# Kernel optimization log

Hardware: AMD Instinct MI355X
Metric: run time of the kernel (lower is better)

The kernel has to match this reference:

```python
import jax, jax.numpy as jnp
import numpy as np

EMBED_DIM = 1024
NUM_HEADS = 16
HEAD_DIM = EMBED_DIM // NUM_HEADS
LN_EPS = 1e-5


def setup_inputs() -> dict:
    key = jax.random.key(0)
    ks = jax.random.split(key, 12)
    B, SQ, SKV, E = 2, 1024, 4096, EMBED_DIM
    s = 1.0 / np.sqrt(E)
    return {
        "query": jax.random.normal(ks[0], (B, SQ, E), jnp.float32),
        "key_value": jax.random.normal(ks[1], (B, SKV, E), jnp.float32),
        "key_value_mask": jax.random.randint(ks[2], (B, SKV), 0, 2, jnp.int32),
        "Wq": jax.random.normal(ks[3], (E, E), jnp.float32) * s,
        "bq": jnp.zeros((E,), jnp.float32),
        "Wk": jax.random.normal(ks[4], (E, E), jnp.float32) * s,
        "bk": jnp.zeros((E,), jnp.float32),
        "Wv": jax.random.normal(ks[5], (E, E), jnp.float32) * s,
        "bv": jnp.zeros((E,), jnp.float32),
        "Wo": jax.random.normal(ks[6], (E, E), jnp.float32) * s,
        "bo": jnp.zeros((E,), jnp.float32),
        "ln_gamma": jnp.ones((E,), jnp.float32),
        "ln_beta": jnp.zeros((E,), jnp.float32),
    }


def reference(query, key_value, key_value_mask, Wq, bq, Wk, bk, Wv, bv, Wo, bo, ln_gamma, ln_beta):
    B, SQ, E = query.shape
    SKV = key_value.shape[1]
    H, D = NUM_HEADS, HEAD_DIM
    # projections (dropout is eval-mode identity)
    q = (query @ Wq.T + bq).reshape(B, SQ, H, D).transpose(0, 2, 1, 3)      # b h sq d
    k = (key_value @ Wk.T + bk).reshape(B, SKV, H, D).transpose(0, 2, 1, 3)  # b h skv d
    v = (key_value @ Wv.T + bv).reshape(B, SKV, H, D).transpose(0, 2, 1, 3)
    scale = jnp.sqrt(jnp.asarray(D, q.dtype))
    scores = jnp.einsum('bhqd,bhkd->bhqk', q, k) / scale                     # b h sq skv
    mask = (key_value_mask != 0)[:, None, None, :]                           # b 1 1 skv
    scores = jnp.where(mask, scores, jnp.asarray(-jnp.inf, scores.dtype))
    attn = jax.nn.softmax(scores, axis=-1)
    out = jnp.einsum('bhqk,bhkd->bhqd', attn, v)
    out = out.transpose(0, 2, 1, 3).reshape(B, SQ, E)
    out = out @ Wo.T + bo
    # post-LN residual
    x = query + out
    mu = jnp.mean(x, axis=-1, keepdims=True)
    var = jnp.mean(jnp.square(x - mu), axis=-1, keepdims=True)
    return (x - mu) * jax.lax.rsqrt(var + LN_EPS) * ln_gamma + ln_beta
```

## Files before the change

kernel.cpp:

```cpp
#include <hip/hip_runtime.h>
#include <cstdint>


typedef __bf16 bf16x8_t  __attribute__((ext_vector_type(8)));
typedef float  f32x4_t   __attribute__((ext_vector_type(4)));
typedef float  f32x16_t  __attribute__((ext_vector_type(16)));

#define E_DIM 1024
#define NH    16
#define HD    64
#define SCALE_L2E 0.1803368804f

__device__ __forceinline__ unsigned short f32_bf16(float f) {
    union { float f; unsigned int u; } v; v.f = f;
    unsigned int u = v.u;
    unsigned int r = (u + 0x7fffu + ((u >> 16) & 1u)) >> 16;
    return (unsigned short)r;
}

__device__ __forceinline__ unsigned pack_bf16(float a, float b) {
    __bf16 x = (__bf16)a, y = (__bf16)b;
    unsigned short ux = __builtin_bit_cast(unsigned short, x);
    unsigned short uy = __builtin_bit_cast(unsigned short, y);
    return (unsigned)ux | ((unsigned)uy << 16);
}

__device__ __forceinline__ void gld16(const unsigned short* g, unsigned short* l) {
    __builtin_amdgcn_global_load_lds(
        (const __attribute__((address_space(1))) unsigned int*)g,
        (__attribute__((address_space(3))) unsigned int*)l, 16, 0, 0);
}

__device__ __forceinline__ bf16x8_t ld16g(const unsigned short* p) {
    union { uint4 u; bf16x8_t f; } v;
    v.u = *reinterpret_cast<const uint4*>(p);
    return v.f;
}

__global__ void cast_all(const float* __restrict__ q, const float* __restrict__ kv,
                         const float* __restrict__ wq, const float* __restrict__ wk,
                         const float* __restrict__ wv, const float* __restrict__ wo,
                         unsigned short* __restrict__ Xq, unsigned short* __restrict__ Xkv,
                         unsigned short* __restrict__ Wqb, unsigned short* __restrict__ Wkb,
                         unsigned short* __restrict__ Wvb, unsigned short* __restrict__ Wob,
                         const int* __restrict__ msk, float* __restrict__ Sub) {
    __shared__ int red[4];
    if (blockIdx.x >= 14336) {
        int b = blockIdx.x - 14336, t = threadIdx.x;
        int s = 0;
#pragma unroll
        for (int k = 0; k < 16; k++) s += (msk[b * 4096 + k * 256 + t] != 0);
#pragma unroll
        for (int off = 32; off >= 1; off >>= 1) s += __shfl_xor(s, off, 64);
        if ((t & 63) == 0) red[t >> 6] = s;
        __syncthreads();
        if (t == 0)
            Sub[b] = (float)(4096 - (red[0] + red[1] + red[2] + red[3]));
        return;
    }
    long i = (long)blockIdx.x * 256 + threadIdx.x;
    const float* src; unsigned short* dst; long off;
    if (i < 2621440) {
        if (i < 524288) { src = q;  dst = Xq;  off = i; }
        else            { src = kv; dst = Xkv; off = i - 524288; }
    } else {
        long j = i - 2621440;
        int w = (int)(j >> 18); off = j & 262143;
        src = (w == 0) ? wq : (w == 1) ? wk : (w == 2) ? wv : wo;
        dst = (w == 0) ? Wqb : (w == 1) ? Wkb : (w == 2) ? Wvb : Wob;
    }
    float4 v = reinterpret_cast<const float4*>(src)[off];
    ushort4 o;
    o.x = f32_bf16(v.x); o.y = f32_bf16(v.y);
    o.z = f32_bf16(v.z); o.w = f32_bf16(v.w);
    reinterpret_cast<ushort4*>(dst)[off] = o;
}

#define BK 64

__global__ __launch_bounds__(256) void gemm_q(
    const unsigned short* __restrict__ A,
    const unsigned short* __restrict__ W,
    const float* __restrict__ bias,
    unsigned short* __restrict__ out)
{
    __shared__ __align__(16) unsigned short As[64 * BK];
    __shared__ __align__(16) unsigned short Bs[128 * BK];
    int tid  = threadIdx.x;
    int m0   = blockIdx.y * 64;
    int n0   = blockIdx.x * 128;
    int lane = tid & 63;
    int wvu  = __builtin_amdgcn_readfirstlane(tid >> 6);
    int l15  = lane & 15, quad = lane >> 4, x7 = l15 & 7;
    int wm   = ((tid >> 6) >> 1) * 32, wn = ((tid >> 6) & 1) * 64;

    f32x4_t acc[2][4];
#pragma unroll
    for (int i = 0; i < 2; i++)
#pragma unroll
        for (int j = 0; j < 4; j++) acc[i][j] = (f32x4_t)(0.f);

    for (int k0 = 0; k0 < 1024; k0 += BK) {
        __syncthreads();
#pragma unroll
        for (int i = 0; i < 2; i++) {
            int s = (i * 4 + wvu) * 64 + lane;
            int row = s >> 3, pcol = ((s & 7) ^ (row & 7)) << 3;
            gld16(&A[(long)(m0 + row) * 1024 + k0 + pcol], &As[(i * 4 + wvu) * 512]);
        }
#pragma unroll
        for (int i = 0; i < 4; i++) {
            int s = (i * 4 + wvu) * 64 + lane;
            int row = s >> 3, pcol = ((s & 7) ^ (row & 7)) << 3;
            gld16(&W[(long)(n0 + row) * 1024 + k0 + pcol], &Bs[(i * 4 + wvu) * 512]);
        }
        __syncthreads();
        const char* Ab = (const char*)As;
        const char* Bb = (const char*)Bs;
#pragma unroll
        for (int ks = 0; ks < 2; ks++) {
            int pos = (((ks << 2) + quad) ^ x7) << 4;
            bf16x8_t af[2], bf[4];
#pragma unroll
            for (int mi = 0; mi < 2; mi++)
                af[mi] = *reinterpret_cast<const bf16x8_t*>(
                    Ab + (wm + mi * 16 + l15) * 128 + pos);
#pragma unroll
            for (int ni = 0; ni < 4; ni++)
                bf[ni] = *reinterpret_cast<const bf16x8_t*>(
                    Bb + (wn + ni * 16 + l15) * 128 + pos);
#pragma unroll
            for (int mi = 0; mi < 2; mi++)
#pragma unroll
                for (int ni = 0; ni < 4; ni++)
                    acc[mi][ni] = __builtin_amdgcn_mfma_f32_16x16x32_bf16(
                        af[mi], bf[ni], acc[mi][ni], 0, 0, 0);
        }
    }
#pragma unroll
    for (int mi = 0; mi < 2; mi++)
#pragma unroll
        for (int ni = 0; ni < 4; ni++) {
            int n = n0 + wn + ni * 16 + l15;
            float bv = bias[n];
            int h = n >> 6, d = n & 63;
#pragma unroll
            for (int r = 0; r < 4; r++) {
                int mg = m0 + wm + mi * 16 + quad * 4 + r;
                int b = mg >> 10, s = mg & 1023;
                out[(((b * NH + h) << 10) + s) * HD + d] =
                    f32_bf16((acc[mi][ni][r] + bv) * SCALE_L2E);
            }
        }
}

__global__ __launch_bounds__(256) void gemm_kv(
    const unsigned short* __restrict__ A,
    const unsigned short* __restrict__ Wk,
    const unsigned short* __restrict__ Wv,
    const float* __restrict__ bk,
    const float* __restrict__ bv,
    unsigned short* __restrict__ Kout,
    unsigned short* __restrict__ Vout,
    const int* __restrict__ kvm)
{
    __shared__ __align__(16) unsigned short As[128 * BK];
    __shared__ __align__(16) unsigned short Bs[128 * BK];
    int tid  = threadIdx.x;
    int bx   = blockIdx.x;
    int isV  = bx >= 8;
    int m0   = blockIdx.y * 128;
    int n0   = (bx & 7) * 128;
    const unsigned short* W = isV ? Wv : Wk;
    const float* bias = isV ? bv : bk;
    int lane = tid & 63;
    int wvu  = __builtin_amdgcn_readfirstlane(tid >> 6);
    int l15  = lane & 15, quad = lane >> 4, x7 = l15 & 7;
    int wm   = ((tid >> 6) >> 1) * 64, wn = ((tid >> 6) & 1) * 64;

    f32x4_t acc[4][4];
#pragma unroll
    for (int i = 0; i < 4; i++)
#pragma unroll
        for (int j = 0; j < 4; j++) acc[i][j] = (f32x4_t)(0.f);

    for (int k0 = 0; k0 < 1024; k0 += BK) {
        __syncthreads();
#pragma unroll
        for (int i = 0; i < 4; i++) {
            int s = (i * 4 + wvu) * 64 + lane;
            int row = s >> 3, pcol = ((s & 7) ^ (row & 7)) << 3;
            gld16(&A[(long)(m0 + row) * 1024 + k0 + pcol], &As[(i * 4 + wvu) * 512]);
            gld16(&W[(long)(n0 + row) * 1024 + k0 + pcol], &Bs[(i * 4 + wvu) * 512]);
        }
        __syncthreads();
        const char* Ab = (const char*)As;
        const char* Bb = (const char*)Bs;
#pragma unroll
        for (int ks = 0; ks < 2; ks++) {
            int pos = (((ks << 2) + quad) ^ x7) << 4;
            bf16x8_t af[4], bf[4];
#pragma unroll
            for (int mi = 0; mi < 4; mi++)
                af[mi] = *reinterpret_cast<const bf16x8_t*>(
                    Ab + (wm + mi * 16 + l15) * 128 + pos);
#pragma unroll
            for (int ni = 0; ni < 4; ni++)
                bf[ni] = *reinterpret_cast<const bf16x8_t*>(
                    Bb + (wn + ni * 16 + l15) * 128 + pos);
#pragma unroll
            for (int mi = 0; mi < 4; mi++)
#pragma unroll
                for (int ni = 0; ni < 4; ni++)
                    acc[mi][ni] = __builtin_amdgcn_mfma_f32_16x16x32_bf16(
                        af[mi], bf[ni], acc[mi][ni], 0, 0, 0);
        }
    }
    int4 mk[4];
#pragma unroll
    for (int mi = 0; mi < 4; mi++) {
        int mg0 = m0 + wm + mi * 16 + quad * 4;
        mk[mi] = *reinterpret_cast<const int4*>(&kvm[mg0]);
    }
    if (!isV) {
#pragma unroll
        for (int mi = 0; mi < 4; mi++)
#pragma unroll
            for (int ni = 0; ni < 4; ni++) {
                int n = n0 + wn + ni * 16 + l15;
                float bvv = bias[n];
                int h = n >> 6, d = n & 63;
#pragma unroll
                for (int r = 0; r < 4; r++) {
                    int mg = m0 + wm + mi * 16 + quad * 4 + r;
                    int b = mg >> 12, s = mg & 4095;
                    unsigned short val = (&mk[mi].x)[r]
                        ? f32_bf16(acc[mi][ni][r] + bvv) : (unsigned short)0;
                    Kout[(((b * NH + h) << 12) + s) * HD + d] = val;
                }
            }
    } else {
#pragma unroll
        for (int mi = 0; mi < 4; mi++)
#pragma unroll
            for (int ni = 0; ni < 4; ni++) {
                int n = n0 + wn + ni * 16 + l15;
                float bvv = bias[n];
                int h = n >> 6, d = n & 63;
                int mg0 = m0 + wm + mi * 16 + quad * 4;
                int b = mg0 >> 12, s = mg0 & 4095;
                ushort4 w;
                w.x = mk[mi].x ? f32_bf16(acc[mi][ni][0] + bvv) : (unsigned short)0;
                w.y = mk[mi].y ? f32_bf16(acc[mi][ni][1] + bvv) : (unsigned short)0;
                w.z = mk[mi].z ? f32_bf16(acc[mi][ni][2] + bvv) : (unsigned short)0;
                w.w = mk[mi].w ? f32_bf16(acc[mi][ni][3] + bvv) : (unsigned short)0;
                *reinterpret_cast<ushort4*>(
                    &Vout[(((b * NH + h) * HD + d) << 12) + s]) = w;
            }
    }
}

__global__ __launch_bounds__(256) void gemm_oproj(
    const unsigned short* __restrict__ A,
    const unsigned short* __restrict__ W,
    const float* __restrict__ bias,
    const float* __restrict__ resid,
    float* __restrict__ xout)
{
    __shared__ __align__(16) unsigned short As[64 * BK];
    __shared__ __align__(16) unsigned short Bs[128 * BK];
    int tid  = threadIdx.x;
    int m0   = blockIdx.y * 64;
    int n0   = blockIdx.x * 128;
    int lane = tid & 63;
    int wvu  = __builtin_amdgcn_readfirstlane(tid >> 6);
    int l15  = lane & 15, quad = lane >> 4, x7 = l15 & 7;
    int wm   = ((tid >> 6) >> 1) * 32, wn = ((tid >> 6) & 1) * 64;

    f32x4_t acc[2][4];
#pragma unroll
    for (int i = 0; i < 2; i++)
#pragma unroll
        for (int j = 0; j < 4; j++) acc[i][j] = (f32x4_t)(0.f);

    for (int k0 = 0; k0 < 1024; k0 += BK) {
        __syncthreads();
#pragma unroll
        for (int i = 0; i < 2; i++) {
            int s = (i * 4 + wvu) * 64 + lane;
            int row = s >> 3, pcol = ((s & 7) ^ (row & 7)) << 3;
            gld16(&A[(long)(m0 + row) * 1024 + k0 + pcol], &As[(i * 4 + wvu) * 512]);
        }
#pragma unroll
        for (int i = 0; i < 4; i++) {
            int s = (i * 4 + wvu) * 64 + lane;
            int row = s >> 3, pcol = ((s & 7) ^ (row & 7)) << 3;
            gld16(&W[(long)(n0 + row) * 1024 + k0 + pcol], &Bs[(i * 4 + wvu) * 512]);
        }
        __syncthreads();
        const char* Ab = (const char*)As;
        const char* Bb = (const char*)Bs;
#pragma unroll
        for (int ks = 0; ks < 2; ks++) {
            int pos = (((ks << 2) + quad) ^ x7) << 4;
            bf16x8_t af[2], bf[4];
#pragma unroll
            for (int mi = 0; mi < 2; mi++)
                af[mi] = *reinterpret_cast<const bf16x8_t*>(
                    Ab + (wm + mi * 16 + l15) * 128 + pos);
#pragma unroll
            for (int ni = 0; ni < 4; ni++)
                bf[ni] = *reinterpret_cast<const bf16x8_t*>(
                    Bb + (wn + ni * 16 + l15) * 128 + pos);
#pragma unroll
            for (int mi = 0; mi < 2; mi++)
#pragma unroll
                for (int ni = 0; ni < 4; ni++)
                    acc[mi][ni] = __builtin_amdgcn_mfma_f32_16x16x32_bf16(
                        af[mi], bf[ni], acc[mi][ni], 0, 0, 0);
        }
    }
#pragma unroll
    for (int mi = 0; mi < 2; mi++)
#pragma unroll
        for (int ni = 0; ni < 4; ni++) {
            int n = n0 + wn + ni * 16 + l15;
            float bv = bias[n];
#pragma unroll
            for (int r = 0; r < 4; r++) {
                int mg = m0 + wm + mi * 16 + quad * 4 + r;
                xout[mg * 1024 + n] = acc[mi][ni][r] + bv + resid[mg * 1024 + n];
            }
        }
}

__global__ __launch_bounds__(256, 4) void attn_kernel(
    const unsigned short* __restrict__ Q,
    const unsigned short* __restrict__ K,
    const unsigned short* __restrict__ VT,
    float* __restrict__ Osc,
    float* __restrict__ Lsc)
{
    __shared__ __align__(16) union {
        struct { unsigned short Kb[2][4096]; unsigned short Vb[2][4096]; } st;
        struct { float OL[2][2048]; float ls[64]; } mg;
    } sm;

    int tid  = threadIdx.x;
    int lane = tid & 63;
    int w    = tid >> 6;
    int wvu  = __builtin_amdgcn_readfirstlane(w);
    int l31  = lane & 31, hw = lane >> 5;
    int qsub = w & 1, kvsub = w >> 1;

    int bid  = blockIdx.x;
    int xcd  = bid & 7, gidx = bid >> 3;
    int bh   = xcd * 4 + (gidx & 3);
    int rest = gidx >> 2;
    int q0   = (rest & 15) * 64;
    int bhalf = rest >> 4;

    const unsigned short* Kb = K + ((long)bh * 4096 + bhalf * 2048) * HD;
    const unsigned short* Vb = VT + (long)bh * HD * 4096 + bhalf * 2048;
    const unsigned short* Qb = Q + ((long)bh * 1024 + q0) * HD;

    bf16x8_t qfr[4];
#pragma unroll
    for (int ks = 0; ks < 4; ks++)
        qfr[ks] = ld16g(Qb + (qsub * 32 + l31) * HD + ks * 16 + hw * 8);

    f32x16_t oacc[2];
    oacc[0] = (f32x16_t)(0.f); oacc[1] = (f32x16_t)(0.f);
    float l_run = 0.f;

    auto stage = [&](int kt, int bufi) {
#pragma unroll
        for (int i = 0; i < 2; i++) {
            int s = (i * 4 + wvu) * 64 + lane;
            int row = s >> 3, pc = ((s & 7) ^ (row & 7)) << 3;
            gld16(&Kb[(long)(kt * 64 + row) * HD + pc], &sm.st.Kb[bufi][(i * 4 + wvu) * 512]);
            gld16(&Vb[(long)row * 4096 + kt * 64 + pc], &sm.st.Vb[bufi][(i * 4 + wvu) * 512]);
        }
    };

    const char* Kc = (const char*)sm.st.Kb;
    const char* Vc = (const char*)sm.st.Vb;

    stage(0, 0);
#pragma unroll 2
    for (int kt = 0; kt < 32; kt++) {
        __syncthreads();
        if (kt + 1 < 32) stage(kt + 1, (kt + 1) & 1);
        int bo = (kt & 1) * 8192;

        f32x16_t sa = (f32x16_t)(0.f);
        int krow = kvsub * 32 + l31;
#pragma unroll
        for (int ks = 0; ks < 4; ks++) {
            int phys = (ks * 2 + hw) ^ (krow & 7);
            bf16x8_t kf = *reinterpret_cast<const bf16x8_t*>(
                Kc + bo + krow * 128 + phys * 16);
            sa = __builtin_amdgcn_mfma_f32_32x32x16_bf16(kf, qfr[ks], sa, 0, 0, 0);
        }

        float pv[16];
        float rs = 0.f;
#pragma unroll
        for (int r = 0; r < 16; r++) {
            pv[r] = exp2f(sa[r]);
            rs += pv[r];
        }
        l_run += rs;
        unsigned pku[8];
#pragma unroll
        for (int s4 = 0; s4 < 4; s4++) {
            pku[s4 * 2 + 0] = pack_bf16(pv[s4 * 4 + 0], pv[s4 * 4 + 1]);
            pku[s4 * 2 + 1] = pack_bf16(pv[s4 * 4 + 2], pv[s4 * 4 + 3]);
        }

#pragma unroll
        for (int ks2 = 0; ks2 < 2; ks2++) {
            int s_lo = ks2 * 2, s_own = ks2 * 2 + hw;
            unsigned send0 = hw ? pku[s_lo * 2 + 0] : pku[(s_lo + 1) * 2 + 0];
            unsigned send1 = hw ? pku[s_lo * 2 + 1] : pku[(s_lo + 1) * 2 + 1];
            unsigned recv0 = __shfl_xor((int)send0, 32, 64);
            unsigned recv1 = __shfl_xor((int)send1, 32, 64);
            union { uint4 u; bf16x8_t f; } bw;
            bw.u.x = hw ? recv0 : pku[s_own * 2 + 0];
            bw.u.y = hw ? recv1 : pku[s_own * 2 + 1];
            bw.u.z = hw ? pku[s_own * 2 + 0] : recv0;
            bw.u.w = hw ? pku[s_own * 2 + 1] : recv1;
            int c = kvsub * 4 + ks2 * 2 + hw;
#pragma unroll
            for (int ds = 0; ds < 2; ds++) {
                int vrow = ds * 32 + l31;
                int phys = c ^ (vrow & 7);
                bf16x8_t va = *reinterpret_cast<const bf16x8_t*>(
                    Vc + bo + vrow * 128 + phys * 16);
                oacc[ds] = __builtin_amdgcn_mfma_f32_32x32x16_bf16(
                    va, bw.f, oacc[ds], 0, 0, 0);
            }
        }
    }

    l_run += __shfl_xor(l_run, 32, 64);
    __syncthreads();
    if (kvsub == 1) {
        float* OL = sm.mg.OL[qsub];
#pragma unroll
        for (int ds = 0; ds < 2; ds++)
#pragma unroll
            for (int r = 0; r < 16; r++) {
                int d = ds * 32 + (r & 3) + 8 * (r >> 2) + 4 * hw;
                OL[d * 32 + l31] = oacc[ds][r];
            }
        if (hw == 0) sm.mg.ls[qsub * 32 + l31] = l_run;
    }
    __syncthreads();
    if (kvsub == 0) {
        const float* OL = sm.mg.OL[qsub];
        int q = q0 + qsub * 32 + l31;
        long obase = (((long)bhalf * 32 + bh) * 64) * 1024;
#pragma unroll
        for (int ds = 0; ds < 2; ds++)
#pragma unroll
            for (int r = 0; r < 16; r++) {
                int d = ds * 32 + (r & 3) + 8 * (r >> 2) + 4 * hw;
                Osc[obase + (long)d * 1024 + q] = oacc[ds][r] + OL[d * 32 + l31];
            }
        if (hw == 0)
            Lsc[((long)bhalf * 32 + bh) * 1024 + q] = l_run + sm.mg.ls[qsub * 32 + l31];
    }
}

__global__ __launch_bounds__(256) void attn_merge(
    const float* __restrict__ Osc, const float* __restrict__ Lsc,
    const float* __restrict__ Sub, unsigned short* __restrict__ AO)
{
    __shared__ unsigned short T[64 * 66];
    int t = threadIdx.x, w = t >> 6, lane = t & 63;
    int bh = blockIdx.y, b = bh >> 4, h = bh & 15;
    int q0 = blockIdx.x * 64;
    int q = q0 + lane;

    float ls = Lsc[(long)bh * 1024 + q]
             + Lsc[(long)(32 + bh) * 1024 + q] - Sub[b];
    float inv = __builtin_amdgcn_rcpf(ls);
    inv = inv * (2.f - ls * inv);

#pragma unroll
    for (int dd = 0; dd < 16; dd++) {
        int d = w * 16 + dd;
        long base = (long)bh * 64 * 1024 + (long)d * 1024 + q;
        float o = Osc[base] + Osc[base + 32l * 64 * 1024];
        T[lane * 66 + d] = f32_bf16(o * inv);
    }
    __syncthreads();
    int q2 = t >> 2, c16 = (t & 3) * 16;
    unsigned ov[8];
#pragma unroll
    for (int j = 0; j < 8; j++)
        ov[j] = *reinterpret_cast<const unsigned*>(&T[q2 * 66 + c16 + j * 2]);
    unsigned short* dst = &AO[((long)(b * 1024 + q0 + q2)) * E_DIM + h * HD + c16];
    reinterpret_cast<uint4*>(dst)[0] = make_uint4(ov[0], ov[1], ov[2], ov[3]);
    reinterpret_cast<uint4*>(dst)[1] = make_uint4(ov[4], ov[5], ov[6], ov[7]);
}

__global__ __launch_bounds__(256) void ln_kernel(
    const float* __restrict__ x, const float* __restrict__ g,
    const float* __restrict__ be, float* __restrict__ out)
{
    __shared__ float red[8];
    int row = blockIdx.x, tid = threadIdx.x;
    float4 v = reinterpret_cast<const float4*>(x)[row * 256 + tid];
    float s  = v.x + v.y + v.z + v.w;
    float sq = v.x * v.x + v.y * v.y + v.z * v.z + v.w * v.w;
#pragma unroll
    for (int off = 32; off >= 1; off >>= 1) {
        s  += __shfl_xor(s,  off, 64);
        sq += __shfl_xor(sq, off, 64);
    }
    if ((tid & 63) == 0) { red[tid >> 6] = s; red[4 + (tid >> 6)] = sq; }
    __syncthreads();
    s  = red[0] + red[1] + red[2] + red[3];
    sq = red[4] + red[5] + red[6] + red[7];
    float mu  = s * (1.f / 1024.f);
    float var = sq * (1.f / 1024.f) - mu * mu;
    float rs  = rsqrtf(var + 1e-5f);
    int c = tid * 4;
    float4 o;
    o.x = (v.x - mu) * rs * g[c]     + be[c];
    o.y = (v.y - mu) * rs * g[c + 1] + be[c + 1];
    o.z = (v.z - mu) * rs * g[c + 2] + be[c + 2];
    o.w = (v.w - mu) * rs * g[c + 3] + be[c + 3];
    reinterpret_cast<float4*>(out)[row * 256 + tid] = o;
}

extern "C" void kernel_launch(void* const* d_in, const int* in_sizes, int n_in,
                              void* d_out, int out_size, void* d_ws, size_t ws_size,
                              hipStream_t stream) {
    const float* query     = (const float*)d_in[0];
    const float* key_value = (const float*)d_in[1];
    const int*   kv_mask   = (const int*)d_in[2];
    const float* Wq = (const float*)d_in[3];
    const float* bq = (const float*)d_in[4];
    const float* Wk = (const float*)d_in[5];
    const float* bk = (const float*)d_in[6];
    const float* Wv = (const float*)d_in[7];
    const float* bv = (const float*)d_in[8];
    const float* Wo = (const float*)d_in[9];
    const float* bo = (const float*)d_in[10];
    const float* ln_g = (const float*)d_in[11];
    const float* ln_b = (const float*)d_in[12];
    float* out = (float*)d_out;

    char* ws = (char*)d_ws;
    unsigned short* Xq  = (unsigned short*)(ws);
    unsigned short* Xkv = (unsigned short*)(ws + (4ll  << 20));
    unsigned short* Wqb = (unsigned short*)(ws + (20ll << 20));
    unsigned short* Wkb = (unsigned short*)(ws + (22ll << 20));
    unsigned short* Wvb = (unsigned short*)(ws + (24ll << 20));
    float*          Osc = (float*)(ws);
    unsigned short* Kh  = (unsigned short*)(ws + (32ll << 20));
    unsigned short* VTh = (unsigned short*)(ws + (48ll << 20));
    unsigned short* AO  = (unsigned short*)(ws + (64ll << 20));
    float*          Xr  = (float*)(ws + (68ll << 20));
    float*          Lsc = (float*)(ws + (76ll << 20));
    float*          Sub = (float*)(ws + (77ll << 20));
    unsigned short* Qh  = (unsigned short*)(ws + (80ll << 20));
    unsigned short* Wob = (unsigned short*)(ws + (84ll << 20));

    cast_all<<<14338, 256, 0, stream>>>(query, key_value, Wq, Wk, Wv, Wo,
                                        Xq, Xkv, Wqb, Wkb, Wvb, Wob,
                                        kv_mask, Sub);

    gemm_kv<<<dim3(16, 64), 256, 0, stream>>>(Xkv, Wkb, Wvb, bk, bv, Kh, VTh, kv_mask);
    gemm_q<<<dim3(8, 32), 256, 0, stream>>>(Xq, Wqb, bq, Qh);

    attn_kernel<<<1024, 256, 0, stream>>>(Qh, Kh, VTh, Osc, Lsc);
    attn_merge<<<dim3(16, 32), 256, 0, stream>>>(Osc, Lsc, Sub, AO);

    gemm_oproj<<<dim3(8, 32), 256, 0, stream>>>(AO, Wob, bo, query, Xr);

    ln_kernel<<<2048, 256, 0, stream>>>(Xr, ln_g, ln_b, out);
}
```

Baseline: 269.0 us.

## Widen attention blocks to 128 queries with 512 threads, permlane swap, priorities

```diff
diff --git a/kernel.cpp b/kernel.cpp
--- a/kernel.cpp
+++ b/kernel.cpp
@@ -334,7 +334,7 @@
         }
 }
 
-__global__ __launch_bounds__(256, 4) void attn_kernel(
+__global__ __launch_bounds__(512, 4) void attn_kernel(
     const unsigned short* __restrict__ Q,
     const unsigned short* __restrict__ K,
     const unsigned short* __restrict__ VT,
@@ -343,7 +343,7 @@
 {
     __shared__ __align__(16) union {
         struct { unsigned short Kb[2][4096]; unsigned short Vb[2][4096]; } st;
-        struct { float OL[2][2048]; float ls[64]; } mg;
+        struct { float OL[4][2048]; float ls[128]; } mg;
     } sm;
 
     int tid  = threadIdx.x;
@@ -351,14 +351,14 @@
     int w    = tid >> 6;
     int wvu  = __builtin_amdgcn_readfirstlane(w);
     int l31  = lane & 31, hw = lane >> 5;
-    int qsub = w & 1, kvsub = w >> 1;
+    int qsub = w & 3, kvsub = w >> 2;
 
     int bid  = blockIdx.x;
     int xcd  = bid & 7, gidx = bid >> 3;
     int bh   = xcd * 4 + (gidx & 3);
     int rest = gidx >> 2;
-    int q0   = (rest & 15) * 64;
-    int bhalf = rest >> 4;
+    int q0   = (rest & 7) * 128;
+    int bhalf = rest >> 3;
 
     const unsigned short* Kb = K + ((long)bh * 4096 + bhalf * 2048) * HD;
     const unsigned short* Vb = VT + (long)bh * HD * 4096 + bhalf * 2048;
@@ -374,13 +374,10 @@
     float l_run = 0.f;
 
     auto stage = [&](int kt, int bufi) {
-#pragma unroll
-        for (int i = 0; i < 2; i++) {
-            int s = (i * 4 + wvu) * 64 + lane;
-            int row = s >> 3, pc = ((s & 7) ^ (row & 7)) << 3;
-            gld16(&Kb[(long)(kt * 64 + row) * HD + pc], &sm.st.Kb[bufi][(i * 4 + wvu) * 512]);
-            gld16(&Vb[(long)row * 4096 + kt * 64 + pc], &sm.st.Vb[bufi][(i * 4 + wvu) * 512]);
-        }
+        int s = wvu * 64 + lane;
+        int row = s >> 3, pc = ((s & 7) ^ (row & 7)) << 3;
+        gld16(&Kb[(long)(kt * 64 + row) * HD + pc], &sm.st.Kb[bufi][wvu * 512]);
+        gld16(&Vb[(long)row * 4096 + kt * 64 + pc], &sm.st.Vb[bufi][wvu * 512]);
     };
 
     const char* Kc = (const char*)sm.st.Kb;
@@ -395,6 +392,7 @@
 
         f32x16_t sa = (f32x16_t)(0.f);
         int krow = kvsub * 32 + l31;
+        __builtin_amdgcn_s_setprio(1);
 #pragma unroll
         for (int ks = 0; ks < 4; ks++) {
             int phys = (ks * 2 + hw) ^ (krow & 7);
@@ -402,15 +400,16 @@
                 Kc + bo + krow * 128 + phys * 16);
             sa = __builtin_amdgcn_mfma_f32_32x32x16_bf16(kf, qfr[ks], sa, 0, 0, 0);
         }
+        __builtin_amdgcn_s_setprio(0);
 
         float pv[16];
-        float rs = 0.f;
-#pragma unroll
-        for (int r = 0; r < 16; r++) {
-            pv[r] = exp2f(sa[r]);
-            rs += pv[r];
-        }
-        l_run += rs;
+#pragma unroll
+        for (int r = 0; r < 16; r++) pv[r] = exp2f(sa[r]);
+        float s0 = (pv[0] + pv[1]) + (pv[2] + pv[3]);
+        float s1 = (pv[4] + pv[5]) + (pv[6] + pv[7]);
+        float s2 = (pv[8] + pv[9]) + (pv[10] + pv[11]);
+        float s3 = (pv[12] + pv[13]) + (pv[14] + pv[15]);
+        l_run += (s0 + s1) + (s2 + s3);
         unsigned pku[8];
 #pragma unroll
         for (int s4 = 0; s4 < 4; s4++) {
@@ -418,18 +417,17 @@
             pku[s4 * 2 + 1] = pack_bf16(pv[s4 * 4 + 2], pv[s4 * 4 + 3]);
         }
 
+        __builtin_amdgcn_s_setprio(1);
 #pragma unroll
         for (int ks2 = 0; ks2 < 2; ks2++) {
-            int s_lo = ks2 * 2, s_own = ks2 * 2 + hw;
-            unsigned send0 = hw ? pku[s_lo * 2 + 0] : pku[(s_lo + 1) * 2 + 0];
-            unsigned send1 = hw ? pku[s_lo * 2 + 1] : pku[(s_lo + 1) * 2 + 1];
-            unsigned recv0 = __shfl_xor((int)send0, 32, 64);
-            unsigned recv1 = __shfl_xor((int)send1, 32, 64);
+            unsigned x0 = pku[(ks2 * 2) * 2 + 0];
+            unsigned x1 = pku[(ks2 * 2) * 2 + 1];
+            unsigned z0 = pku[(ks2 * 2 + 1) * 2 + 0];
+            unsigned z1 = pku[(ks2 * 2 + 1) * 2 + 1];
+            asm("v_permlane32_swap_b32 %0, %1" : "+v"(x0), "+v"(z0));
+            asm("v_permlane32_swap_b32 %0, %1" : "+v"(x1), "+v"(z1));
             union { uint4 u; bf16x8_t f; } bw;
-            bw.u.x = hw ? recv0 : pku[s_own * 2 + 0];
-            bw.u.y = hw ? recv1 : pku[s_own * 2 + 1];
-            bw.u.z = hw ? pku[s_own * 2 + 0] : recv0;
-            bw.u.w = hw ? pku[s_own * 2 + 1] : recv1;
+            bw.u.x = x0; bw.u.y = x1; bw.u.z = z0; bw.u.w = z1;
             int c = kvsub * 4 + ks2 * 2 + hw;
 #pragma unroll
             for (int ds = 0; ds < 2; ds++) {
@@ -441,6 +439,7 @@
                     va, bw.f, oacc[ds], 0, 0, 0);
             }
         }
+        __builtin_amdgcn_s_setprio(0);
     }
 
     l_run += __shfl_xor(l_run, 32, 64);
@@ -577,7 +576,7 @@
     gemm_kv<<<dim3(16, 64), 256, 0, stream>>>(Xkv, Wkb, Wvb, bk, bv, Kh, VTh, kv_mask);
     gemm_q<<<dim3(8, 32), 256, 0, stream>>>(Xq, Wqb, bq, Qh);
 
-    attn_kernel<<<1024, 256, 0, stream>>>(Qh, Kh, VTh, Osc, Lsc);
+    attn_kernel<<<512, 512, 0, stream>>>(Qh, Kh, VTh, Osc, Lsc);
     attn_merge<<<dim3(16, 32), 256, 0, stream>>>(Osc, Lsc, Sub, AO);
 
     gemm_oproj<<<dim3(8, 32), 256, 0, stream>>>(AO, Wob, bo, query, Xr);
```

Measured after the change: 258.0 us. -4.1%, faster.
